# Optimization experiments

Measured on AMD Instinct MI355X. Metric: run time of the kernel, lower is better.

## Reference

```python
import jax, jax.numpy as jnp
import numpy as np

B, L_PROG = 8, 12
NUM_CLASSES, NUM_ATTRS = 256, 256
MAX_CONCEPTS, MAX_OBJECTS = 4096, 128
N_ATTR_PER_OBJ = 8
E, A, H = 64, 64, 256  # embed_dim, attention_dim, hidden_dim


def setup_inputs() -> dict:
    key = jax.random.key(0)
    ks = jax.random.split(key, 22)
    f = lambda k, shape: jax.random.normal(k, shape, dtype=jnp.float32) * 0.05
    return {
        'class_embIn': f(ks[0], (NUM_CLASSES, E)),
        'class_embOut': f(ks[1], (NUM_CLASSES, E)),
        'attr_embIn': f(ks[2], (NUM_ATTRS, E)),
        'attr_embOut': f(ks[3], (NUM_ATTRS, E)),
        'concept_embIn': f(ks[4], (MAX_CONCEPTS, E)),
        'concept_embOut': f(ks[5], (MAX_CONCEPTS, E)),
        'meta_init': f(ks[6], (A,)),
        'object_init': f(ks[7], (E,)),
        'attention_init': f(ks[8], (A,)),
        'axon_w1': f(ks[9], (A + E, H)), 'axon_b1': f(ks[10], (H,)),
        'axon_w2': f(ks[11], (H, E)), 'axon_b2': f(ks[12], (E,)),
        'meta_w1': f(ks[13], (E + A, H)), 'meta_b1': f(ks[14], (H,)),
        'meta_w2': f(ks[15], (H, A)), 'meta_b2': f(ks[16], (A,)),
        'program_ops': jax.random.randint(ks[17], (B, L_PROG), 0, 3),
        'program_args': jax.random.randint(ks[18], (B, L_PROG), 0, MAX_CONCEPTS),
        'gt_classes': jax.random.randint(ks[19], (B, MAX_OBJECTS), 0, NUM_CLASSES),
        'gt_attributes': jax.random.randint(ks[20], (B, MAX_OBJECTS, N_ATTR_PER_OBJ), 0, NUM_ATTRS),
    }


def _mlp(x, w1, b1, w2, b2):
    return jnp.maximum(x @ w1 + b1, 0.0) @ w2 + b2


def reference(class_embIn, class_embOut, attr_embIn, attr_embOut,
              concept_embIn, concept_embOut, meta_init, object_init,
              attention_init, axon_w1, axon_b1, axon_w2, axon_b2,
              meta_w1, meta_b1, meta_w2, meta_b2,
              program_ops, program_args, gt_classes, gt_attributes):
    Bb, Lp = program_ops.shape
    C = concept_embIn.shape[0]
    N = C + gt_classes.shape[1]  # dim_concept = max_concepts + max_objects

    # object embeddings: class embedding + sum of attribute embeddings  (B, O, E)
    objIn = class_embIn[gt_classes] + attr_embIn[gt_attributes].sum(axis=2)
    objOut = class_embOut[gt_classes] + attr_embOut[gt_attributes].sum(axis=2)

    # thought = [concepts ; objects]  (B, N, E)
    thoughtIn = jnp.concatenate(
        [jnp.broadcast_to(concept_embIn[None], (Bb, C, E)), objIn], axis=1)
    thoughtOut = jnp.concatenate(
        [jnp.broadcast_to(concept_embOut[None], (Bb, C, E)), objOut], axis=1)

    args_emb = concept_embOut[program_args]          # (B, L, E)
    is_mode = (program_ops == 0).astype(jnp.float32)     # (B, L)
    is_insert = (program_ops == 1).astype(jnp.float32)
    is_transfer = (program_ops == 2).astype(jnp.float32)

    meta0 = jnp.broadcast_to(meta_init[None], (Bb, A))
    att0 = jnp.broadcast_to(attention_init[None, None], (Bb, N, A))

    def step(carry, xs):
        meta, attention = carry
        m, ins, tr, arg = xs  # (B,), (B,), (B,), (B,E)
        new_meta = _mlp(jnp.concatenate([meta, arg], axis=-1),
                        meta_w1, meta_b1, meta_w2, meta_b2)
        meta = m[:, None] * new_meta + (1.0 - m[:, None]) * meta
        # insert: meta scaled by mean_e(arg * thoughtOut)
        proj = (arg[:, None, :] * thoughtOut).mean(axis=-1)        # (B, N)
        att_insert = meta[:, None, :] * proj[:, :, None]           # (B, N, A)
        # transfer: bilinear scores thoughtIn . axon, mean-aggregate attention
        mb = jnp.broadcast_to(meta[:, None, :], (Bb, N, A))
        axon = _mlp(jnp.concatenate([thoughtOut, mb], axis=-1),
                    axon_w1, axon_b1, axon_w2, axon_b2)            # (B, N, E)
        scores = jnp.einsum('bje,bke->bjk', thoughtIn, axon)       # (B, N, N)
        att_transfer = jnp.einsum('bjk,bka->bja', scores, attention) / N
        attention = attention + ins[:, None, None] * att_insert \
                              + tr[:, None, None] * att_transfer
        return (meta, attention), None

    xs = (is_mode.T, is_insert.T, is_transfer.T,
          jnp.transpose(args_emb, (1, 0, 2)))
    (meta, attention), _ = jax.lax.scan(step, (meta0, att0), xs)

    output_length = jnp.mean(attention ** 2, axis=-1)              # (B, N)
    return jax.nn.log_softmax(output_length, axis=1)
```

## Files before the change

kernel.cpp:

```cpp
#include <hip/hip_runtime.h>
#include <hip/hip_bf16.h>

typedef __hip_bfloat16 bf16;
typedef float f32x4 __attribute__((ext_vector_type(4)));
typedef short s16x8 __attribute__((ext_vector_type(8)));

#define B_    8
#define LP    12
#define NC    4096
#define NO    128
#define NAPO  8
#define NN    4224
#define E_    64
#define A_    64
#define H_    256
#define QC    80
#define PROJ0 65
#define NCHUNK 17

#define TOT_IN 688896
#define QTF_C  67584
#define QTF_B  337920
#define TB_P   983040

struct Ptr16 { const void* p[16]; };
union U8 { s16x8 v; unsigned u[4]; };

__device__ __forceinline__ float b2f(bf16 x){ return __bfloat162float(x); }
__device__ __forceinline__ float bs2f(unsigned short s){
  union { unsigned u; float f; } x; x.u = ((unsigned)s) << 16; return x.f;
}
__device__ __forceinline__ unsigned short f2bs(float f){
  bf16 h = __float2bfloat16(f);
  union { bf16 h; unsigned short s; } x; x.h = h; return x.s;
}
__device__ __forceinline__ unsigned pack2(float a, float b){
  return (unsigned)f2bs(a) | ((unsigned)f2bs(b) << 16);
}
__device__ __forceinline__ float lo16f(unsigned w){
  union { unsigned u; float f; } x; x.u = w << 16; return x.f;
}
__device__ __forceinline__ float hi16f(unsigned w){
  union { unsigned u; float f; } x; x.u = w & 0xffff0000u; return x.f;
}
__device__ __forceinline__ float rdval(const void* p, int i, int fl){
  return fl ? ((const float*)p)[i] : bs2f(((const unsigned short*)p)[i]);
}

__global__ void k_prep(Ptr16 ps, int* flag, float* dst,
                       unsigned short* awFrag,
                       const int* gtc, const int* gta,
                       float* objIn, float* objOut, float* qsum_esum){
  int tid = threadIdx.x;
  const unsigned short* u = (const unsigned short*)ps.p[4];
  int hit = (((u[tid*16] >> 7) & 0xFF) >= 137) ? 1 : 0;
  unsigned long long m = __ballot(hit);
  int fl = (m != 0ULL) ? 1 : 0;
  int mb = blockIdx.x;
  if (mb < 673){
    int idx = (mb*256 + tid)*4;
    if (idx >= TOT_IN) return;
    constexpr int cum[17] = {0,16384,32768,49152,65536,327680,589824,589888,589952,
                             622720,622976,639360,639424,672192,672448,688832,688896};
    int t = 0;
    #pragma unroll
    for (int i=1;i<16;i++) if (idx >= cum[i]) t = i;
    int off = idx - cum[t];
    float4 v;
    if (fl){
      v = *(const float4*)((const float*)ps.p[t] + off);
    } else {
      uint2 sv = *(const uint2*)((const unsigned short*)ps.p[t] + off);
      v.x = lo16f(sv.x); v.y = hi16f(sv.x);
      v.z = lo16f(sv.y); v.w = hi16f(sv.y);
    }
    *(float4*)(dst + idx) = v;
  } else if (mb < 737){
    int idx = (mb-673)*256 + tid;
    int j = idx & 7;
    int lane = (idx >> 3) & 63;
    int mm = (idx >> 9) & 15;
    int kc = idx >> 13;
    int e = kc*32 + (lane>>4)*8 + j;
    int h = mm*16 + (lane&15);
    awFrag[idx] = f2bs(rdval(ps.p[8], e*H_ + h, fl));
  } else if (mb < 993){
    int idx = (mb-737)*256 + tid;
    int e = idx & 63; int bo = idx >> 6;
    int cls = gtc[bo];
    float vi = rdval(ps.p[0], cls*E_ + e, fl);
    float vo = rdval(ps.p[1], cls*E_ + e, fl);
    const int* ga = gta + bo*NAPO;
    #pragma unroll
    for (int j=0;j<NAPO;j++){
      int at = ga[j];
      vi += rdval(ps.p[2], at*E_ + e, fl);
      vo += rdval(ps.p[3], at*E_ + e, fl);
    }
    objIn[idx] = vi; objOut[idx] = vo;
  } else {
    if (tid < 656) qsum_esum[tid] = 0.f;
    if (tid == 0) *flag = fl;
  }
}

__device__ __forceinline__ void mid_meta(char* smem, int b,
                       const float* conceptOut, const float* meta_init,
                       const float* mw1, const float* mb1, const float* mw2, const float* mb2,
                       const float* aw1, const float* ab1,
                       const int* ops, const int* args,
                       float* metaAll, float* metaH){
  unsigned* mw1p = (unsigned*)smem;
  unsigned* mw2p = (unsigned*)(smem + 65536);
  unsigned* aw1p = (unsigned*)(smem + 98304);
  float* meta_s  = (float*)(smem + 131072);
  float* argx    = (float*)(smem + 131328);
  float* hid     = (float*)(smem + 131584);
  float* part    = (float*)(smem + 132608);
  int tid = threadIdx.x;

  for (int i=tid; i<64*256; i+=256){
    int j2 = i >> 8, t = i & 255;
    mw1p[i] = pack2(mw1[(2*j2)*H_ + t], mw1[(2*j2+1)*H_ + t]);
  }
  for (int i=tid; i<128*64; i+=256){
    int h2 = i >> 6, a = i & 63;
    mw2p[i] = pack2(mw2[(2*h2)*A_ + a], mw2[(2*h2+1)*A_ + a]);
  }
  for (int i=tid; i<32*256; i+=256){
    int a2 = i >> 8, t = i & 255;
    aw1p[i] = pack2(aw1[(E_+2*a2)*H_ + t], aw1[(E_+2*a2+1)*H_ + t]);
  }
  float r_mb1 = mb1[tid];
  float r_ab1 = ab1[tid];
  float r_mb2 = (tid < A_) ? mb2[tid] : 0.f;
  if (tid < A_) meta_s[tid] = meta_init[tid];
  __syncthreads();

  float mh = r_ab1;
  for (int a2=0;a2<32;a2++){
    unsigned w = aw1p[a2*256 + tid];
    float2 mp = *(const float2*)&meta_s[2*a2];
    mh = fmaf(mp.x, lo16f(w), mh);
    mh = fmaf(mp.y, hi16f(w), mh);
  }

  for (int t=0;t<LP;t++){
    int op  = ops[b*LP + t];
    if (op == 0){
      int arg = args[b*LP + t];
      if (tid >= 64 && tid < 128) argx[tid-64] = conceptOut[arg*E_ + (tid-64)];
      __syncthreads();
      float acc = r_mb1;
      for (int j2=0;j2<32;j2++){
        unsigned w = mw1p[j2*256 + tid];
        float2 xp = *(const float2*)&meta_s[2*j2];
        acc = fmaf(xp.x, lo16f(w), acc);
        acc = fmaf(xp.y, hi16f(w), acc);
      }
      for (int j2=0;j2<32;j2++){
        unsigned w = mw1p[(32+j2)*256 + tid];
        float2 xp = *(const float2*)&argx[2*j2];
        acc = fmaf(xp.x, lo16f(w), acc);
        acc = fmaf(xp.y, hi16f(w), acc);
      }
      hid[tid] = fmaxf(acc, 0.f);
      __syncthreads();
      int wv_ = tid >> 6, l = tid & 63;
      float acc2 = 0.f;
      for (int h2 = wv_*32; h2 < wv_*32+32; h2++){
        unsigned w = mw2p[h2*64 + l];
        float2 hp = *(const float2*)&hid[2*h2];
        acc2 = fmaf(hp.x, lo16f(w), acc2);
        acc2 = fmaf(hp.y, hi16f(w), acc2);
      }
      part[wv_*64 + l] = acc2;
      __syncthreads();
      if (tid < A_){
        float s = part[tid] + part[64+tid] + part[128+tid] + part[192+tid] + r_mb2;
        meta_s[tid] = s;
      }
      __syncthreads();
      mh = r_ab1;
      for (int a2=0;a2<32;a2++){
        unsigned w = aw1p[a2*256 + tid];
        float2 mp = *(const float2*)&meta_s[2*a2];
        mh = fmaf(mp.x, lo16f(w), mh);
        mh = fmaf(mp.y, hi16f(w), mh);
      }
    }
    if (tid < A_) metaAll[(b*LP+t)*A_ + tid] = meta_s[tid];
    metaH[(b*LP+t)*H_ + tid] = mh;
  }
}

__device__ __forceinline__ void mid_qt(char* smem, int idx,
                       const float* conceptIn, const float* conceptOut, const int* args,
                       const float* objIn, const float* objOut,
                       unsigned short* QTf, float* qsum){
  float* tile = (float*)smem;
  float* argv = (float*)(smem + 66560);
  float* qs   = (float*)(smem + 69632);
  int b = idx / NCHUNK, chunk = idx % NCHUNK;
  int tid = threadIdx.x;
  int rows = (chunk < 16) ? 256 : 128;
  int n0 = chunk*256;
  int n = n0 + tid;
  bool valid = (tid < rows);
  if (tid < 80) qs[tid] = 0.f;
  unsigned short* Qb = QTf + (size_t)b*QTF_B + ((n>>5)*512 + (n&31));
  {
    const float* src = (chunk < 16) ? (conceptIn + (size_t)n0*E_) : (objIn + (size_t)b*NO*E_);
    int tot = rows*64;
    for (int i=tid; i<tot; i+=256) tile[(i>>6)*65 + (i&63)] = src[i];
  }
  __syncthreads();
  if (valid){
    Qb[0] = 0x3F80;
    Qb[4*QTF_C + 13*32] = 0;
    Qb[4*QTF_C + 14*32] = 0;
    Qb[4*QTF_C + 15*32] = 0;
    for (int e=0;e<64;e++){
      int qc = 1+e;
      Qb[(qc>>4)*QTF_C + (qc&15)*32] = f2bs(tile[tid*65 + e]);
    }
    for (int i=0;i<64;i++){
      int e = (i + tid) & 63;
      atomicAdd(&qs[1+e], tile[tid*65+e]);
    }
  }
  __syncthreads();
  for (int i=tid;i<LP*E_;i+=256) argv[i] = conceptOut[args[b*LP + (i>>6)]*E_ + (i&63)];
  {
    const float* src = (chunk < 16) ? (conceptOut + (size_t)n0*E_) : (objOut + (size_t)b*NO*E_);
    int tot = rows*64;
    for (int i=tid; i<tot; i+=256) tile[(i>>6)*65 + (i&63)] = src[i];
  }
  __syncthreads();
  float dots[LP];
  #pragma unroll
  for (int t=0;t<LP;t++) dots[t] = 0.f;
  for (int e=0;e<64;e++){
    float o = tile[tid*65 + e];
    #pragma unroll
    for (int t=0;t<LP;t++) dots[t] += o*argv[t*64+e];
  }
  #pragma unroll
  for (int t=0;t<LP;t++){
    float v = valid ? dots[t]*(1.f/E_) : 0.f;
    if (valid){
      int qc = PROJ0+t;
      Qb[(qc>>4)*QTF_C + (qc&15)*32] = f2bs(v);
    }
    float r = v;
    #pragma unroll
    for (int off=32; off>0; off>>=1) r += __shfl_down(r, off, 64);
    if ((tid & 63) == 0) atomicAdd(&qs[PROJ0+t], r);
  }
  __syncthreads();
  if (tid < 80) atomicAdd(&qsum[b*QC + tid], qs[tid]);
  if (chunk == 0 && tid == 0) atomicAdd(&qsum[b*QC], (float)NN);
}

__device__ __forceinline__ void mid_base(int blk,
                       const float* conceptOut, const float* objOut,
                       const unsigned short* awFrag,
                       unsigned short* AoptC, unsigned short* AoptO){
  int n0 = blk * 64;
  int tid = threadIdx.x;
  int w = tid >> 6, l = tid & 63, quad = l >> 4, lq = l & 15;
  int n = n0 + w*16 + lq;
  const float* src = (n < NC) ? (conceptOut + (size_t)n*E_) : (objOut + (size_t)(n-NC)*E_);
  f32x4 acc[16];
  #pragma unroll
  for (int m=0;m<16;m++) acc[m] = (f32x4){0.f,0.f,0.f,0.f};
  #pragma unroll
  for (int kc=0;kc<2;kc++){
    s16x8 bfr;
    #pragma unroll
    for (int j=0;j<8;j++) bfr[j] = (short)f2bs(src[kc*32 + quad*8 + j]);
    const unsigned short* ap = awFrag + ((size_t)(kc*16)*64 + l)*8;
    #pragma unroll
    for (int m=0;m<16;m++){
      s16x8 af = *(const s16x8*)(ap + (size_t)m*64*8);
      acc[m] = __builtin_amdgcn_mfma_f32_16x16x32_bf16(af, bfr, acc[m], 0, 0, 0);
    }
  }
  int nl = n & 31;
  if (n < NC){
    int nch = n >> 5;
    #pragma unroll
    for (int m=0;m<16;m++){
      #pragma unroll
      for (int r=0;r<4;r++)
        AoptC[(size_t)(m*128 + nch)*512 + (quad*4+r)*32 + nl] = f2bs(acc[m][r]);
    }
  } else {
    int no = n - NC; int bb = no >> 7; int oc = (no & 127) >> 5;
    #pragma unroll
    for (int m=0;m<16;m++){
      #pragma unroll
      for (int r=0;r<4;r++)
        AoptO[(size_t)((bb*16 + m)*4 + oc)*512 + (quad*4+r)*32 + nl] = f2bs(acc[m][r]);
    }
  }
}

__global__ __launch_bounds__(256) void k_mid(
    const float* conceptIn, const float* conceptOut,
    const float* meta_init, const float* mw1, const float* mb1, const float* mw2, const float* mb2,
    const float* aw1, const float* ab1, const int* ops, const int* args,
    const float* objIn, const float* objOut, const unsigned short* awFrag,
    float* metaAll, float* metaH, unsigned short* QTf, float* qsum,
    unsigned short* AoptC, unsigned short* AoptO){
  __shared__ __align__(16) char smem[133888];
  int mb = blockIdx.x;
  if (mb < 8)
    mid_meta(smem, mb, conceptOut, meta_init, mw1, mb1, mw2, mb2, aw1, ab1, ops, args, metaAll, metaH);
  else if (mb < 144)
    mid_qt(smem, mb-8, conceptIn, conceptOut, args, objIn, objOut, QTf, qsum);
  else
    mid_base(mb-144, conceptOut, objOut, awFrag, AoptC, AoptO);
}

__global__ __launch_bounds__(64) void k_T(const unsigned short* AoptC, const unsigned short* AoptO,
                                          const unsigned short* QTf, const float* metaH,
                                          const int* ops, unsigned* TB){
  int bid = blockIdx.x;
  int kh = bid & 7; int ht = (bid >> 3) & 3; int bt = bid >> 5; int b = bt / LP;
  if (ops[bt] != 2) return;
  int l = threadIdx.x, quad = l >> 4, lq = l & 15;
  int off = lq*32 + quad*8;
  int start = (kh < 4) ? (kh*17) : (68 + (kh-4)*16);
  int count = (kh < 4) ? 17 : 16;
  float mh[4];
  #pragma unroll
  for (int s=0;s<4;s++) mh[s] = metaH[(size_t)bt*H_ + ht*64 + s*16 + lq];
  f32x4 acc[4][5];
  #pragma unroll
  for (int s=0;s<4;s++){
    #pragma unroll
    for (int c=0;c<5;c++) acc[s][c] = (f32x4){0.f,0.f,0.f,0.f};
  }
  const unsigned short* QTb = QTf + (size_t)b*QTF_B + off;
  const unsigned short* AC  = AoptC + (size_t)(ht*4)*65536 + off;
  const unsigned short* AO  = AoptO + (size_t)(b*16 + ht*4)*2048 + off;
  for (int it=0; it<count; it++){
    int nchunk = start + it;
    U8 bfr[5];
    #pragma unroll
    for (int c=0;c<5;c++)
      bfr[c].v = *(const s16x8*)(QTb + (size_t)c*QTF_C + (size_t)nchunk*512);
    bool isC = (nchunk < 128);
    #pragma unroll
    for (int s=0;s<4;s++){
      U8 a;
      a.v = isC ? *(const s16x8*)(AC + (size_t)s*65536 + (size_t)nchunk*512)
                : *(const s16x8*)(AO + (size_t)s*2048 + (size_t)(nchunk-128)*512);
      float mhs = mh[s];
      U8 af;
      #pragma unroll
      for (int d=0;d<4;d++){
        unsigned wv = a.u[d];
        float lo = fmaxf(__uint_as_float(wv << 16) + mhs, 0.f);
        float hi = fmaxf(__uint_as_float(wv & 0xffff0000u) + mhs, 0.f);
        af.u[d] = __builtin_amdgcn_perm(__float_as_uint(hi), __float_as_uint(lo), 0x07060302u);
      }
      #pragma unroll
      for (int c=0;c<5;c++)
        acc[s][c] = __builtin_amdgcn_mfma_f32_16x16x32_bf16(af.v, bfr[c].v, acc[s][c], 0, 0, 0);
    }
  }
  unsigned* Tp = TB + (size_t)kh*TB_P + ((size_t)bt*4 + ht)*2560;
  #pragma unroll
  for (int s=0;s<4;s++){
    #pragma unroll
    for (int c=0;c<5;c++){
      uint2 v;
      v.x = pack2(acc[s][c][0], acc[s][c][1]);
      v.y = pack2(acc[s][c][2], acc[s][c][3]);
      *(uint2*)(Tp + (s*5+c)*128 + l*2) = v;
    }
  }
}

__global__ __launch_bounds__(256) void k_U(const unsigned* TB,
                                           const float* w2, const float* b2v,
                                           const float* qsum, const int* ops,
                                           float* Ut0, float* Ut1){
  __shared__ float Wt[128*64];
  __shared__ float Tt[128*81];
  int bid = blockIdx.x;
  int kq = bid & 1; int bt = bid >> 1; int b = bt / LP;
  if (ops[bt] != 2) return;
  int tid = threadIdx.x;
  for (int i=tid; i<8192; i+=256){
    int hl = i >> 6, e = i & 63;
    Wt[i] = w2[(kq*128 + hl)*E_ + e];
  }
  #pragma unroll
  for (int half=0; half<2; half++){
    const unsigned* base = TB + ((size_t)bt*4 + kq*2 + half)*2560;
    for (int i2=tid; i2<2560; i2+=256){
      float lo = 0.f, hi = 0.f;
      #pragma unroll
      for (int p=0;p<8;p++){
        unsigned w = base[(size_t)p*TB_P + i2];
        lo += lo16f(w); hi += hi16f(w);
      }
      int idx = 2*i2;
      int sc = idx >> 8; int ll = (idx >> 2) & 63; int r = idx & 3;
      int s = sc/5, c = sc - s*5;
      int hl = half*64 + s*16 + ((ll>>4)<<2) + r;
      int qc = c*16 + (ll&15);
      Tt[hl*81 + qc]     = lo;
      Tt[(hl+1)*81 + qc] = hi;
    }
  }
  __syncthreads();
  int el = tid & 15, ql = tid >> 4;
  float acc[4][5];
  #pragma unroll
  for (int i=0;i<4;i++){
    #pragma unroll
    for (int j=0;j<5;j++) acc[i][j]=0.f;
  }
  #pragma unroll 4
  for (int kk=0; kk<128; kk++){
    float4 wv = *(const float4*)&Wt[kk*64 + el*4];
    float ww[4] = {wv.x, wv.y, wv.z, wv.w};
    const float* tp = &Tt[kk*81 + ql*5];
    #pragma unroll
    for (int j=0;j<5;j++){
      float tv = tp[j];
      #pragma unroll
      for (int i=0;i<4;i++) acc[i][j] = fmaf(ww[i], tv, acc[i][j]);
    }
  }
  const float invN = 1.f/NN;
  float* Up = (kq ? Ut1 : Ut0) + (size_t)bt*5120;
  if (kq == 0){
    float be[4], qv[5];
    #pragma unroll
    for (int i=0;i<4;i++) be[i] = b2v[el*4+i];
    #pragma unroll
    for (int j=0;j<5;j++) qv[j] = qsum[b*QC + ql*5+j];
    #pragma unroll
    for (int i=0;i<4;i++){
      #pragma unroll
      for (int j=0;j<5;j++)
        Up[(el*4+i)*QC + ql*5+j] = (acc[i][j] + be[i]*qv[j]) * invN;
    }
  } else {
    #pragma unroll
    for (int i=0;i<4;i++){
      #pragma unroll
      for (int j=0;j<5;j++)
        Up[(el*4+i)*QC + ql*5+j] = acc[i][j] * invN;
    }
  }
}

__global__ __launch_bounds__(256) void k_rec(const float* Ut0, const float* Ut1, const float* metaAll,
                                             const int* ops, const float* att_init, float* Cm){
  __shared__ float C[QC*65];
  __shared__ float Ul[2][64*81];
  int b = blockIdx.x, tid = threadIdx.x;
  int w = tid >> 6, l = tid & 63, quad = l >> 4, lq = l & 15;
  for (int i=tid;i<QC*65;i+=256) C[i] = 0.f;
  if (tid < A_) C[tid] = att_init[tid];
  if (ops[b*LP] == 2){
    const float* U0 = Ut0 + (size_t)(b*LP)*5120;
    const float* U1 = Ut1 + (size_t)(b*LP)*5120;
    #pragma unroll
    for (int k=0;k<5;k++){
      int i = tid*4 + k*1024;
      float4 v0 = *(const float4*)&U0[i];
      float4 v1 = *(const float4*)&U1[i];
      int r = i/80, c = i%80;
      Ul[0][r*81+c]   = v0.x+v1.x; Ul[0][r*81+c+1] = v0.y+v1.y;
      Ul[0][r*81+c+2] = v0.z+v1.z; Ul[0][r*81+c+3] = v0.w+v1.w;
    }
  }
  __syncthreads();
  for (int t=0;t<LP;t++){
    int opn = (t < LP-1) ? ops[b*LP + t + 1] : 0;
    float4 rv0[5], rv1[5];
    if (opn == 2){
      const float* U0 = Ut0 + (size_t)(b*LP+t+1)*5120;
      const float* U1 = Ut1 + (size_t)(b*LP+t+1)*5120;
      #pragma unroll
      for (int k=0;k<5;k++){
        rv0[k] = *(const float4*)&U0[tid*4 + k*1024];
        rv1[k] = *(const float4*)&U1[tid*4 + k*1024];
      }
    }
    int op = ops[b*LP + t];
    f32x4 acc[4];
    if (op == 2){
      const float* Uc = Ul[t&1];
      U8 af[3][4];
      #pragma unroll
      for (int k0t=0;k0t<3;k0t++){
        #pragma unroll
        for (int s=0;s<4;s++){
          int e = s*16 + lq;
          int qb = k0t*32 + quad*8;
          float v[8];
          #pragma unroll
          for (int j=0;j<8;j++){
            int qc = qb + j;
            v[j] = (qc < QC) ? Uc[e*81 + qc] : 0.f;
          }
          #pragma unroll
          for (int d=0;d<4;d++) af[k0t][s].u[d] = pack2(v[2*d], v[2*d+1]);
        }
      }
      U8 bf[3];
      #pragma unroll
      for (int k0t=0;k0t<3;k0t++){
        int kb = k0t*32 + quad*8;
        float v[8];
        #pragma unroll
        for (int j=0;j<8;j++){
          int k = kb + j;
          v[j] = (k < QC) ? C[k*65 + w*16 + lq] : 0.f;
        }
        #pragma unroll
        for (int d=0;d<4;d++) bf[k0t].u[d] = pack2(v[2*d], v[2*d+1]);
      }
      #pragma unroll
      for (int s=0;s<4;s++){
        acc[s] = (f32x4){0.f,0.f,0.f,0.f};
        #pragma unroll
        for (int k0t=0;k0t<3;k0t++)
          acc[s] = __builtin_amdgcn_mfma_f32_16x16x32_bf16(af[k0t][s].v, bf[k0t].v, acc[s], 0, 0, 0);
      }
    }
    __syncthreads();
    if (op == 2){
      #pragma unroll
      for (int s=0;s<4;s++){
        #pragma unroll
        for (int r=0;r<4;r++){
          int e = s*16 + quad*4 + r;
          C[(1+e)*65 + w*16 + lq] += acc[s][r];
        }
      }
    } else if (op == 1){
      if (tid < A_) C[(PROJ0+t)*65 + tid] += metaAll[(b*LP+t)*A_ + tid];
    }
    if (opn == 2){
      float* Un = Ul[(t+1)&1];
      #pragma unroll
      for (int k=0;k<5;k++){
        int i = tid*4 + k*1024;
        int r = i/80, c = i%80;
        Un[r*81+c]   = rv0[k].x+rv1[k].x; Un[r*81+c+1] = rv0[k].y+rv1[k].y;
        Un[r*81+c+2] = rv0[k].z+rv1[k].z; Un[r*81+c+3] = rv0[k].w+rv1[k].w;
      }
    }
    __syncthreads();
  }
  for (int i=tid;i<QC*A_;i+=256) Cm[b*QC*A_ + i] = C[(i>>6)*65 + (i&63)];
}

__global__ __launch_bounds__(256) void k_out(const unsigned short* QTf, const float* Cm,
                                             float* ol, float* esum){
  __shared__ float Cpad[QC*65];
  __shared__ float wsum[4];
  int b = blockIdx.x / 66, rem = blockIdx.x % 66;
  int tid = threadIdx.x;
  int w = tid >> 6, l = tid & 63, quad = l >> 4, lq = l & 15;
  for (int i=tid; i<QC*A_; i+=256) Cpad[(i>>6)*65 + (i&63)] = Cm[b*QC*A_ + i];
  __syncthreads();
  U8 bfr[3][4];
  #pragma unroll
  for (int kk=0;kk<3;kk++){
    #pragma unroll
    for (int at=0;at<4;at++){
      float v[8];
      #pragma unroll
      for (int jj=0;jj<8;jj++){
        int j = kk*32 + quad*8 + jj;
        v[jj] = (j < QC) ? Cpad[j*65 + at*16 + lq] : 0.f;
      }
      #pragma unroll
      for (int d=0;d<4;d++) bfr[kk][at].u[d] = pack2(v[2*d], v[2*d+1]);
    }
  }
  const unsigned short* Qb = QTf + (size_t)b*QTF_B;
  int mt = rem*4 + w;
  int nb = (mt>>1)*512 + (mt&1)*16 + lq;
  f32x4 acc[4];
  #pragma unroll
  for (int at=0;at<4;at++) acc[at] = (f32x4){0.f,0.f,0.f,0.f};
  #pragma unroll
  for (int kk=0;kk<3;kk++){
    U8 af;
    #pragma unroll
    for (int d=0;d<4;d++){
      int j0 = kk*32 + quad*8 + 2*d;
      int j1 = j0 + 1;
      unsigned u0 = (j0 < QC) ? (unsigned)Qb[(j0>>4)*QTF_C + (j0&15)*32 + nb] : 0u;
      unsigned u1 = (j1 < QC) ? (unsigned)Qb[(j1>>4)*QTF_C + (j1&15)*32 + nb] : 0u;
      af.u[d] = u0 | (u1 << 16);
    }
    #pragma unroll
    for (int at=0;at<4;at++)
      acc[at] = __builtin_amdgcn_mfma_f32_16x16x32_bf16(af.v, bfr[kk][at].v, acc[at], 0, 0, 0);
  }
  float le = 0.f;
  #pragma unroll
  for (int r=0;r<4;r++){
    float s = 0.f;
    #pragma unroll
    for (int at=0;at<4;at++) s = fmaf(acc[at][r], acc[at][r], s);
    s += __shfl_xor(s, 1, 64);
    s += __shfl_xor(s, 2, 64);
    s += __shfl_xor(s, 4, 64);
    s += __shfl_xor(s, 8, 64);
    if (lq == 0){
      float o = s * (1.f/A_);
      ol[(size_t)b*NN + mt*16 + quad*4 + r] = o;
      le += expf(o);
    }
  }
  le += __shfl_down(le, 32, 64);
  le += __shfl_down(le, 16, 64);
  if (l == 0) wsum[w] = le;
  __syncthreads();
  if (tid == 0) atomicAdd(&esum[b], wsum[0]+wsum[1]+wsum[2]+wsum[3]);
}

__global__ void k_fin(const float* ol, const float* esum, const int* flag, void* out){
  int idx = blockIdx.x*256 + threadIdx.x;
  if (idx < B_*NN){
    int b = idx / NN;
    float v = ol[idx] - logf(esum[b]);
    if (*flag) ((float*)out)[idx] = v;
    else       ((bf16*)out)[idx]  = __float2bfloat16(v);
  }
}

extern "C" void kernel_launch(void* const* d_in, const int* in_sizes, int n_in,
                              void* d_out, int out_size, void* d_ws, size_t ws_size,
                              hipStream_t stream) {
  (void)in_sizes; (void)n_in; (void)out_size; (void)ws_size;
  const int* ops  = (const int*)d_in[17];
  const int* args = (const int*)d_in[18];
  const int* gtc  = (const int*)d_in[19];
  const int* gta  = (const int*)d_in[20];

  float* ws = (float*)d_ws;
  int* flag = (int*)ws;
  float* W  = ws + 16;

  const float* conceptIn  = W + 65536;
  const float* conceptOut = W + 327680;
  const float* meta_init  = W + 589824;
  const float* att_init   = W + 589888;
  const float* aw1        = W + 589952;
  const float* ab1        = W + 622720;
  const float* aw2        = W + 622976;
  const float* ab2        = W + 639360;
  const float* mw1        = W + 639424;
  const float* mb1        = W + 672192;
  const float* mw2        = W + 672448;
  const float* mb2        = W + 688832;

  constexpr size_t OFF_OBJIN   = 16 + TOT_IN;
  constexpr size_t OFF_OBJOUT  = OFF_OBJIN  + 65536;
  constexpr size_t OFF_METAALL = OFF_OBJOUT + 65536;
  constexpr size_t OFF_METAH   = OFF_METAALL + 6144;
  constexpr size_t OFF_QSUM    = OFF_METAH  + 24576;
  constexpr size_t OFF_ESUM    = OFF_QSUM   + 640;
  constexpr size_t OFF_UT0     = OFF_ESUM   + 16;
  constexpr size_t OFF_UT1     = OFF_UT0    + 491520;
  constexpr size_t OFF_CM      = OFF_UT1    + 491520;
  constexpr size_t OFF_OL      = OFF_CM     + 40960;
  constexpr size_t OFF_QTF     = OFF_OL     + 33792;
  constexpr size_t OFF_AOPTC   = OFF_QTF    + 1351680;
  constexpr size_t OFF_AOPTO   = OFF_AOPTC  + 524288;
  constexpr size_t OFF_AWF     = OFF_AOPTO  + 131072;
  constexpr size_t OFF_TB      = OFF_AWF    + 8192;

  float* objIn   = ws + OFF_OBJIN;
  float* objOut  = ws + OFF_OBJOUT;
  float* metaAll = ws + OFF_METAALL;
  float* metaH   = ws + OFF_METAH;
  float* qsum    = ws + OFF_QSUM;
  float* esum    = ws + OFF_ESUM;
  float* Ut0     = ws + OFF_UT0;
  float* Ut1     = ws + OFF_UT1;
  float* Cm      = ws + OFF_CM;
  float* ol      = ws + OFF_OL;
  unsigned short* QTf    = (unsigned short*)(ws + OFF_QTF);
  unsigned short* AoptC  = (unsigned short*)(ws + OFF_AOPTC);
  unsigned short* AoptO  = (unsigned short*)(ws + OFF_AOPTO);
  unsigned short* awFrag = (unsigned short*)(ws + OFF_AWF);
  unsigned* TB           = (unsigned*)(ws + OFF_TB);

  Ptr16 ps;
  const int src_idx[16] = {0,1,2,3,4,5,6,8,9,10,11,12,13,14,15,16};
  for (int i=0;i<16;i++) ps.p[i] = d_in[src_idx[i]];

  k_prep<<<994, 256, 0, stream>>>(ps, flag, W, awFrag, gtc, gta, objIn, objOut, qsum);
  k_mid <<<224, 256, 0, stream>>>(conceptIn, conceptOut, meta_init, mw1, mb1, mw2, mb2,
                                  aw1, ab1, ops, args, objIn, objOut, awFrag,
                                  metaAll, metaH, QTf, qsum, AoptC, AoptO);
  k_T   <<<B_*LP*4*8, 64, 0, stream>>>(AoptC, AoptO, QTf, metaH, ops, TB);
  k_U   <<<B_*LP*2, 256, 0, stream>>>(TB, aw2, ab2, qsum, ops, Ut0, Ut1);
  k_rec <<<B_, 256, 0, stream>>>(Ut0, Ut1, metaAll, ops, att_init, Cm);
  k_out <<<B_*66, 256, 0, stream>>>(QTf, Cm, ol, esum);
  k_fin <<<(B_*NN + 255)/256, 256, 0, stream>>>(ol, esum, flag, d_out);
}
```

Baseline: 220.9 us.

## Read concept tables directly from inputs and replace shared atomics with column sums

The prep kernel no longer converts and copies the two large concept embedding tables into the workspace. The mid kernel now reads them straight from the raw inputs, handling either fp32 or bf16 through the runtime flag, and loads bf16 fragments directly when the input is already bf16. The per-element shared-memory atomicAdd column sums become a partitioned column reduction, and the projection reduction is skipped for steps whose op is not an insert. This removes a large copy pass and shrinks the prep grid, at the cost of extra dtype branching in the mid kernel.

```diff
diff --git a/kernel.cpp b/kernel.cpp
--- a/kernel.cpp
+++ b/kernel.cpp
@@ -43,7 +43,7 @@
 __device__ __forceinline__ float hi16f(unsigned w){
   union { unsigned u; float f; } x; x.u = w & 0xffff0000u; return x.f;
 }
-__device__ __forceinline__ float rdval(const void* p, int i, int fl){
+__device__ __forceinline__ float rdval(const void* p, size_t i, int fl){
   return fl ? ((const float*)p)[i] : bs2f(((const unsigned short*)p)[i]);
 }
 
@@ -57,9 +57,10 @@
   unsigned long long m = __ballot(hit);
   int fl = (m != 0ULL) ? 1 : 0;
   int mb = blockIdx.x;
-  if (mb < 673){
-    int idx = (mb*256 + tid)*4;
-    if (idx >= TOT_IN) return;
+  if (mb < 161){
+    int qi = mb*256 + tid;
+    if (qi >= 41152) return;
+    int idx = (qi < 16384) ? qi*4 : qi*4 + 524288;
     constexpr int cum[17] = {0,16384,32768,49152,65536,327680,589824,589888,589952,
                              622720,622976,639360,639424,672192,672448,688832,688896};
     int t = 0;
@@ -75,27 +76,27 @@
       v.z = lo16f(sv.y); v.w = hi16f(sv.y);
     }
     *(float4*)(dst + idx) = v;
-  } else if (mb < 737){
-    int idx = (mb-673)*256 + tid;
+  } else if (mb < 225){
+    int idx = (mb-161)*256 + tid;
     int j = idx & 7;
     int lane = (idx >> 3) & 63;
     int mm = (idx >> 9) & 15;
     int kc = idx >> 13;
     int e = kc*32 + (lane>>4)*8 + j;
     int h = mm*16 + (lane&15);
-    awFrag[idx] = f2bs(rdval(ps.p[8], e*H_ + h, fl));
-  } else if (mb < 993){
-    int idx = (mb-737)*256 + tid;
+    awFrag[idx] = f2bs(rdval(ps.p[8], (size_t)e*H_ + h, fl));
+  } else if (mb < 481){
+    int idx = (mb-225)*256 + tid;
     int e = idx & 63; int bo = idx >> 6;
     int cls = gtc[bo];
-    float vi = rdval(ps.p[0], cls*E_ + e, fl);
-    float vo = rdval(ps.p[1], cls*E_ + e, fl);
+    float vi = rdval(ps.p[0], (size_t)cls*E_ + e, fl);
+    float vo = rdval(ps.p[1], (size_t)cls*E_ + e, fl);
     const int* ga = gta + bo*NAPO;
     #pragma unroll
     for (int j=0;j<NAPO;j++){
       int at = ga[j];
-      vi += rdval(ps.p[2], at*E_ + e, fl);
-      vo += rdval(ps.p[3], at*E_ + e, fl);
+      vi += rdval(ps.p[2], (size_t)at*E_ + e, fl);
+      vo += rdval(ps.p[3], (size_t)at*E_ + e, fl);
     }
     objIn[idx] = vi; objOut[idx] = vo;
   } else {
@@ -104,8 +105,8 @@
   }
 }
 
-__device__ __forceinline__ void mid_meta(char* smem, int b,
-                       const float* conceptOut, const float* meta_init,
+__device__ __forceinline__ void mid_meta(char* smem, int b, int fl, const void* coRaw,
+                       const float* meta_init,
                        const float* mw1, const float* mb1, const float* mw2, const float* mb2,
                        const float* aw1, const float* ab1,
                        const int* ops, const int* args,
@@ -149,7 +150,7 @@
     int op  = ops[b*LP + t];
     if (op == 0){
       int arg = args[b*LP + t];
-      if (tid >= 64 && tid < 128) argx[tid-64] = conceptOut[arg*E_ + (tid-64)];
+      if (tid >= 64 && tid < 128) argx[tid-64] = rdval(coRaw, (size_t)arg*E_ + (tid-64), fl);
       __syncthreads();
       float acc = r_mb1;
       for (int j2=0;j2<32;j2++){
@@ -194,13 +195,14 @@
   }
 }
 
-__device__ __forceinline__ void mid_qt(char* smem, int idx,
-                       const float* conceptIn, const float* conceptOut, const int* args,
-                       const float* objIn, const float* objOut,
+__device__ __forceinline__ void mid_qt(char* smem, int idx, int fl,
+                       const void* ciRaw, const void* coRaw, const int* args,
+                       const float* objIn, const float* objOut, const int* ops,
                        unsigned short* QTf, float* qsum){
   float* tile = (float*)smem;
   float* argv = (float*)(smem + 66560);
   float* qs   = (float*)(smem + 69632);
+  float* colp = (float*)(smem + 69952);
   int b = idx / NCHUNK, chunk = idx % NCHUNK;
   int tid = threadIdx.x;
   int rows = (chunk < 16) ? 256 : 128;
@@ -210,9 +212,13 @@
   if (tid < 80) qs[tid] = 0.f;
   unsigned short* Qb = QTf + (size_t)b*QTF_B + ((n>>5)*512 + (n&31));
   {
-    const float* src = (chunk < 16) ? (conceptIn + (size_t)n0*E_) : (objIn + (size_t)b*NO*E_);
     int tot = rows*64;
-    for (int i=tid; i<tot; i+=256) tile[(i>>6)*65 + (i&63)] = src[i];
+    if (chunk < 16){
+      for (int i=tid; i<tot; i+=256) tile[(i>>6)*65 + (i&63)] = rdval(ciRaw, (size_t)n0*E_ + i, fl);
+    } else {
+      const float* src = objIn + (size_t)b*NO*E_;
+      for (int i=tid; i<tot; i+=256) tile[(i>>6)*65 + (i&63)] = src[i];
+    }
   }
   __syncthreads();
   if (valid){
@@ -224,17 +230,25 @@
       int qc = 1+e;
       Qb[(qc>>4)*QTF_C + (qc&15)*32] = f2bs(tile[tid*65 + e]);
     }
-    for (int i=0;i<64;i++){
-      int e = (i + tid) & 63;
-      atomicAdd(&qs[1+e], tile[tid*65+e]);
-    }
-  }
-  __syncthreads();
-  for (int i=tid;i<LP*E_;i+=256) argv[i] = conceptOut[args[b*LP + (i>>6)]*E_ + (i&63)];
+  }
   {
-    const float* src = (chunk < 16) ? (conceptOut + (size_t)n0*E_) : (objOut + (size_t)b*NO*E_);
+    int col = tid & 63, rg = tid >> 6;
+    float s = 0.f;
+    int r0 = rg*64; int r1 = r0+64; if (r1 > rows) r1 = rows;
+    for (int r=r0; r<r1; r++) s += tile[r*65 + col];
+    colp[rg*64 + col] = s;
+  }
+  __syncthreads();
+  if (tid < 64) qs[1+tid] = colp[tid] + colp[64+tid] + colp[128+tid] + colp[192+tid];
+  for (int i=tid;i<LP*E_;i+=256) argv[i] = rdval(coRaw, (size_t)args[b*LP + (i>>6)]*E_ + (i&63), fl);
+  {
     int tot = rows*64;
-    for (int i=tid; i<tot; i+=256) tile[(i>>6)*65 + (i&63)] = src[i];
+    if (chunk < 16){
+      for (int i=tid; i<tot; i+=256) tile[(i>>6)*65 + (i&63)] = rdval(coRaw, (size_t)n0*E_ + i, fl);
+    } else {
+      const float* src = objOut + (size_t)b*NO*E_;
+      for (int i=tid; i<tot; i+=256) tile[(i>>6)*65 + (i&63)] = src[i];
+    }
   }
   __syncthreads();
   float dots[LP];
@@ -247,38 +261,52 @@
   }
   #pragma unroll
   for (int t=0;t<LP;t++){
-    float v = valid ? dots[t]*(1.f/E_) : 0.f;
+    int opt = ops[b*LP + t];
+    float v = (valid && opt == 1) ? dots[t]*(1.f/E_) : 0.f;
     if (valid){
       int qc = PROJ0+t;
       Qb[(qc>>4)*QTF_C + (qc&15)*32] = f2bs(v);
     }
-    float r = v;
-    #pragma unroll
-    for (int off=32; off>0; off>>=1) r += __shfl_down(r, off, 64);
-    if ((tid & 63) == 0) atomicAdd(&qs[PROJ0+t], r);
+    if (opt == 1){
+      float r = v;
+      #pragma unroll
+      for (int off=32; off>0; off>>=1) r += __shfl_down(r, off, 64);
+      if ((tid & 63) == 0) atomicAdd(&qs[PROJ0+t], r);
+    }
   }
   __syncthreads();
   if (tid < 80) atomicAdd(&qsum[b*QC + tid], qs[tid]);
   if (chunk == 0 && tid == 0) atomicAdd(&qsum[b*QC], (float)NN);
 }
 
-__device__ __forceinline__ void mid_base(int blk,
-                       const float* conceptOut, const float* objOut,
+__device__ __forceinline__ void mid_base(int blk, int fl, const void* coRaw,
+                       const float* objOut,
                        const unsigned short* awFrag,
                        unsigned short* AoptC, unsigned short* AoptO){
   int n0 = blk * 64;
   int tid = threadIdx.x;
   int w = tid >> 6, l = tid & 63, quad = l >> 4, lq = l & 15;
   int n = n0 + w*16 + lq;
-  const float* src = (n < NC) ? (conceptOut + (size_t)n*E_) : (objOut + (size_t)(n-NC)*E_);
   f32x4 acc[16];
   #pragma unroll
   for (int m=0;m<16;m++) acc[m] = (f32x4){0.f,0.f,0.f,0.f};
   #pragma unroll
   for (int kc=0;kc<2;kc++){
     s16x8 bfr;
-    #pragma unroll
-    for (int j=0;j<8;j++) bfr[j] = (short)f2bs(src[kc*32 + quad*8 + j]);
+    size_t eoff = (size_t)0 + kc*32 + quad*8;
+    if (n < NC){
+      if (fl){
+        const float* src = (const float*)coRaw + (size_t)n*E_;
+        #pragma unroll
+        for (int j=0;j<8;j++) bfr[j] = (short)f2bs(src[eoff + j]);
+      } else {
+        bfr = *(const s16x8*)((const unsigned short*)coRaw + (size_t)n*E_ + eoff);
+      }
+    } else {
+      const float* src = objOut + (size_t)(n-NC)*E_;
+      #pragma unroll
+      for (int j=0;j<8;j++) bfr[j] = (short)f2bs(src[eoff + j]);
+    }
     const unsigned short* ap = awFrag + ((size_t)(kc*16)*64 + l)*8;
     #pragma unroll
     for (int m=0;m<16;m++){
@@ -307,20 +335,23 @@
 }
 
 __global__ __launch_bounds__(256) void k_mid(
-    const float* conceptIn, const float* conceptOut,
+    Ptr16 ps, const int* flag,
     const float* meta_init, const float* mw1, const float* mb1, const float* mw2, const float* mb2,
     const float* aw1, const float* ab1, const int* ops, const int* args,
     const float* objIn, const float* objOut, const unsigned short* awFrag,
     float* metaAll, float* metaH, unsigned short* QTf, float* qsum,
     unsigned short* AoptC, unsigned short* AoptO){
   __shared__ __align__(16) char smem[133888];
+  int fl = *flag;
+  const void* ciRaw = ps.p[4];
+  const void* coRaw = ps.p[5];
   int mb = blockIdx.x;
   if (mb < 8)
-    mid_meta(smem, mb, conceptOut, meta_init, mw1, mb1, mw2, mb2, aw1, ab1, ops, args, metaAll, metaH);
+    mid_meta(smem, mb, fl, coRaw, meta_init, mw1, mb1, mw2, mb2, aw1, ab1, ops, args, metaAll, metaH);
   else if (mb < 144)
-    mid_qt(smem, mb-8, conceptIn, conceptOut, args, objIn, objOut, QTf, qsum);
+    mid_qt(smem, mb-8, fl, ciRaw, coRaw, args, objIn, objOut, ops, QTf, qsum);
   else
-    mid_base(mb-144, conceptOut, objOut, awFrag, AoptC, AoptO);
+    mid_base(mb-144, fl, coRaw, objOut, awFrag, AoptC, AoptO);
 }
 
 __global__ __launch_bounds__(64) void k_T(const unsigned short* AoptC, const unsigned short* AoptO,
@@ -656,8 +687,6 @@
   int* flag = (int*)ws;
   float* W  = ws + 16;
 
-  const float* conceptIn  = W + 65536;
-  const float* conceptOut = W + 327680;
   const float* meta_init  = W + 589824;
   const float* att_init   = W + 589888;
   const float* aw1        = W + 589952;
@@ -705,8 +734,8 @@
   const int src_idx[16] = {0,1,2,3,4,5,6,8,9,10,11,12,13,14,15,16};
   for (int i=0;i<16;i++) ps.p[i] = d_in[src_idx[i]];
 
-  k_prep<<<994, 256, 0, stream>>>(ps, flag, W, awFrag, gtc, gta, objIn, objOut, qsum);
-  k_mid <<<224, 256, 0, stream>>>(conceptIn, conceptOut, meta_init, mw1, mb1, mw2, mb2,
+  k_prep<<<482, 256, 0, stream>>>(ps, flag, W, awFrag, gtc, gta, objIn, objOut, qsum);
+  k_mid <<<224, 256, 0, stream>>>(ps, flag, meta_init, mw1, mb1, mw2, mb2,
                                   aw1, ab1, ops, args, objIn, objOut, awFrag,
                                   metaAll, metaH, QTf, qsum, AoptC, AoptO);
   k_T   <<<B_*LP*4*8, 64, 0, stream>>>(AoptC, AoptO, QTf, metaH, ops, TB);
```

Result: slower. 229.9 us (+4.1%).
